# Optimization experiments

Hardware: AMD Instinct MI355X
Metric: run time of the kernel (lower is better)

The kernel has to match this reference:

```python
import jax, jax.numpy as jnp
import numpy as np

B, NUM_TAGS, SEQ_LEN, HIDDEN = 8, 1024, 4096, 256
BLOCK = SEQ_LEN // NUM_TAGS  # tokens per tag block


def setup_inputs() -> dict:
    key = jax.random.key(0)
    k1, k2 = jax.random.split(key)
    inputs = jax.random.normal(k1, (B, SEQ_LEN, HIDDEN), dtype=jnp.float32)
    # Structured tag->token mask: tag i covers token block i and (overlapping) block i+1,
    # mimicking nested HTML tags; the suffix-subtraction in the module resolves overlaps.
    tag_idx = jnp.arange(NUM_TAGS)[:, None]           # [T,1]
    tok_blk = jnp.arange(SEQ_LEN)[None, :] // BLOCK   # [1,S]
    mask = ((tok_blk == tag_idx) | (tok_blk == tag_idx + 1)).astype(jnp.float32)
    tag_to_token = jnp.broadcast_to(mask, (B, NUM_TAGS, SEQ_LEN))
    seq_emb = jax.random.normal(k2, (NUM_TAGS, HIDDEN), dtype=jnp.float32) * 0.02
    return {"inputs": inputs, "tag_to_token": tag_to_token, "seq_emb": seq_emb}


def _deduce_direct_string(tag_to_token):
    # Binary indicator of positive entries
    binm = (tag_to_token > 0).astype(tag_to_token.dtype)          # [B,T,S]
    # Exclusive suffix sum over the tag axis (rows below i), replacing the Python loop
    suffix_incl = jnp.flip(jnp.cumsum(jnp.flip(binm, axis=1), axis=1), axis=1)
    temp = binm - (suffix_incl - binm)                            # bin[i] - sum_{j>i} bin[j]
    temp = jnp.maximum(temp, 0.0)                                 # temp[temp<=0]=0
    # Row-normalize over tokens; empty rows divide by 1
    s = jnp.sum(temp, axis=2, keepdims=True)
    return temp / jnp.where(s == 0, 1.0, s)


def reference(inputs, tag_to_token, seq_emb):
    modified = _deduce_direct_string(tag_to_token)                # [B,T,S]
    out = jnp.einsum('bts,bsh->bth', modified, inputs)            # [B,T,H]
    num_tags = out.shape[1]
    return out + seq_emb[None, :num_tags, :]
```

## Files before the change

### kernel.cpp

```cpp
#include <hip/hip_runtime.h>

#define B_ 8
#define T_ 1024
#define S_ 4096
#define H_ 256

#define STRIP 64
#define CHUNK 128

__global__ void __launch_bounds__(256) colmax_pipe_kernel(const float* __restrict__ ttt,
                                                          int* __restrict__ L,
                                                          int2* __restrict__ range) {
    __shared__ unsigned long long wmask[2][4];
    __shared__ int red[4][STRIP];
    const int strippos = blockIdx.x >> 3;
    const int b  = blockIdx.x & 7;
    const int s0 = strippos * STRIP;
    const int w    = threadIdx.x >> 6;
    const int lane = threadIdx.x & 63;

    const float* colbase = ttt + (size_t)b * T_ * S_ + s0 + lane;

    int best = -1;
    int par = 0;
    float v[32], vn[32];

    {
        const float* p = colbase + (size_t)(T_ - CHUNK + w * 32) * S_;
#pragma unroll
        for (int j = 0; j < 32; ++j)
            v[j] = p[(size_t)j * S_];
    }

    for (int thi = T_; thi > 0; thi -= CHUNK) {
        const int t0 = thi - CHUNK + w * 32;
        if (thi > CHUNK) {
            const float* pn = colbase + (size_t)(t0 - CHUNK) * S_;
#pragma unroll
            for (int j = 0; j < 32; ++j)
                vn[j] = pn[(size_t)j * S_];
        }
        int lm = -1;
#pragma unroll
        for (int j = 0; j < 32; ++j)
            if (v[j] > 0.0f) lm = t0 + j;
        best = max(best, lm);

        wmask[par][w] = __ballot(best >= 0);
        __syncthreads();
        unsigned long long all = wmask[par][0] | wmask[par][1]
                               | wmask[par][2] | wmask[par][3];
        if (all == ~0ull) break;
        par ^= 1;
#pragma unroll
        for (int j = 0; j < 32; ++j)
            v[j] = vn[j];
    }

    red[w][lane] = best;
    __syncthreads();
    if (threadIdx.x < STRIP) {
        const int tid = threadIdx.x;
        int m = max(max(red[0][tid], red[1][tid]),
                    max(red[2][tid], red[3][tid]));
        L[b * S_ + s0 + tid] = m;
        int mn = (m < 0) ? 0x7fffffff : m;
        int mx = m;
#pragma unroll
        for (int k = 32; k >= 1; k >>= 1) {
            mn = min(mn, __shfl_xor(mn, k));
            mx = max(mx, __shfl_xor(mx, k));
        }
        if (tid == 0) {
            int2 rg = {mn, mx};
            range[b * (S_ / STRIP) + strippos] = rg;
        }
    }
}

__global__ void __launch_bounds__(256) gather_range_kernel(const float* __restrict__ inputs,
                                                           const int* __restrict__ L,
                                                           const int2* __restrict__ range,
                                                           const float* __restrict__ seq_emb,
                                                           float* __restrict__ out) {
    const int wid  = threadIdx.x >> 6;
    const int lane = threadIdx.x & 63;
    const int bt = blockIdx.x * 4 + wid;
    const int b = bt >> 10;
    const int t = bt & (T_ - 1);

    const float4* in4 = reinterpret_cast<const float4*>(inputs);

    int2 rg = range[b * (S_ / STRIP) + lane];
    unsigned long long smask = __ballot(rg.x <= t && t <= rg.y);

    float4 acc = {0.0f, 0.0f, 0.0f, 0.0f};
    int c = 0;

    while (smask) {
        int strip = __ffsll(smask) - 1; smask &= smask - 1;
        int Lv = L[b * S_ + strip * STRIP + lane];
        unsigned long long bm = __ballot(Lv == t);
        while (bm) {
            int l = __ffsll(bm) - 1; bm &= bm - 1;
            int s = strip * STRIP + l;
            float4 r = in4[(size_t)(b * S_ + s) * (H_ / 4) + lane];
            acc.x += r.x; acc.y += r.y; acc.z += r.z; acc.w += r.w; c++;
        }
    }

    float inv = (c > 0) ? (1.0f / (float)c) : 0.0f;
    float4 e = reinterpret_cast<const float4*>(seq_emb)[t * (H_ / 4) + lane];
    float4 o;
    o.x = acc.x * inv + e.x;
    o.y = acc.y * inv + e.y;
    o.z = acc.z * inv + e.z;
    o.w = acc.w * inv + e.w;
    reinterpret_cast<float4*>(out)[(size_t)bt * (H_ / 4) + lane] = o;
}

extern "C" void kernel_launch(void* const* d_in, const int* in_sizes, int n_in,
                              void* d_out, int out_size, void* d_ws, size_t ws_size,
                              hipStream_t stream) {
    const float* inputs  = (const float*)d_in[0];
    const float* ttt     = (const float*)d_in[1];
    const float* seq_emb = (const float*)d_in[2];
    float* out = (float*)d_out;

    int* L = (int*)d_ws;
    int2* range = (int2*)(L + B_ * S_);

    colmax_pipe_kernel<<<B_ * (S_ / STRIP), 256, 0, stream>>>(ttt, L, range);

    gather_range_kernel<<<B_ * T_ / 4, 256, 0, stream>>>(inputs, L, range, seq_emb, out);
}
```

Measured before the change: 28.57 us.

## Fuse column-max and gather kernels with inter-block flag synchronization

Merges the column-scan kernel and the gather kernel into a single launch of 512 blocks. Each block first computes last-positive-tag indices for one strip and publishes the strip range, then sets a per-block flag with release semantics. It then waits on the flags of all strips for its batch before gathering 16 output rows. This removes a kernel launch and the dependency gap between the two kernels. In exchange it relies on all blocks being co-resident, or it deadlocks. The flags are never reset, so on repeated calls the wait passes at once and can read stale L and range values from the previous call.

```diff
diff --git a/kernel.cpp b/kernel.cpp
--- a/kernel.cpp
+++ b/kernel.cpp
@@ -7,116 +7,140 @@
 
 #define STRIP 64
 #define CHUNK 128
+#define NSTRIP (S_ / STRIP)
+#define MAGICF 0x5F3759DFu
 
-__global__ void __launch_bounds__(256) colmax_pipe_kernel(const float* __restrict__ ttt,
-                                                          int* __restrict__ L,
-                                                          int2* __restrict__ range) {
+__global__ void __launch_bounds__(256) fused_flag_kernel(
+    const float* __restrict__ inputs,
+    const float* __restrict__ ttt,
+    const float* __restrict__ seq_emb,
+    float* __restrict__ out,
+    int* __restrict__ L,
+    int2* __restrict__ range,
+    unsigned int* __restrict__ flag) {
+
     __shared__ unsigned long long wmask[2][4];
     __shared__ int red[4][STRIP];
-    const int strippos = blockIdx.x >> 3;
-    const int b  = blockIdx.x & 7;
-    const int s0 = strippos * STRIP;
     const int w    = threadIdx.x >> 6;
     const int lane = threadIdx.x & 63;
 
-    const float* colbase = ttt + (size_t)b * T_ * S_ + s0 + lane;
+    {
+        const int strippos = blockIdx.x >> 3;
+        const int b  = blockIdx.x & 7;
+        const int s0 = strippos * STRIP;
+        const float* colbase = ttt + (size_t)b * T_ * S_ + s0 + lane;
 
-    int best = -1;
-    int par = 0;
-    float v[32], vn[32];
+        int best = -1;
+        int par = 0;
+        float v[32], vn[32];
 
-    {
-        const float* p = colbase + (size_t)(T_ - CHUNK + w * 32) * S_;
+        {
+            const float* p = colbase + (size_t)(T_ - CHUNK + w * 32) * S_;
 #pragma unroll
-        for (int j = 0; j < 32; ++j)
-            v[j] = p[(size_t)j * S_];
-    }
+            for (int j = 0; j < 32; ++j) v[j] = p[(size_t)j * S_];
+        }
 
-    for (int thi = T_; thi > 0; thi -= CHUNK) {
-        const int t0 = thi - CHUNK + w * 32;
-        if (thi > CHUNK) {
-            const float* pn = colbase + (size_t)(t0 - CHUNK) * S_;
+        for (int thi = T_; thi > 0; thi -= CHUNK) {
+            const int t0 = thi - CHUNK + w * 32;
+            if (thi > CHUNK) {
+                const float* pn = colbase + (size_t)(t0 - CHUNK) * S_;
+#pragma unroll
+                for (int j = 0; j < 32; ++j) vn[j] = pn[(size_t)j * S_];
+            }
+            int lm = -1;
 #pragma unroll
             for (int j = 0; j < 32; ++j)
-                vn[j] = pn[(size_t)j * S_];
+                if (v[j] > 0.0f) lm = t0 + j;
+            best = max(best, lm);
+
+            wmask[par][w] = __ballot(best >= 0);
+            __syncthreads();
+            unsigned long long all = wmask[par][0] | wmask[par][1]
+                                   | wmask[par][2] | wmask[par][3];
+            if (all == ~0ull) break;
+            par ^= 1;
+#pragma unroll
+            for (int j = 0; j < 32; ++j) v[j] = vn[j];
         }
-        int lm = -1;
+
+        red[w][lane] = best;
+        __syncthreads();
+        if (threadIdx.x < STRIP) {
+            const int tid = threadIdx.x;
+            int m = max(max(red[0][tid], red[1][tid]),
+                        max(red[2][tid], red[3][tid]));
+            L[b * S_ + s0 + tid] = m;
+            int mn = (m < 0) ? 0x7fffffff : m;
+            int mx = m;
 #pragma unroll
-        for (int j = 0; j < 32; ++j)
-            if (v[j] > 0.0f) lm = t0 + j;
-        best = max(best, lm);
-
-        wmask[par][w] = __ballot(best >= 0);
-        __syncthreads();
-        unsigned long long all = wmask[par][0] | wmask[par][1]
-                               | wmask[par][2] | wmask[par][3];
-        if (all == ~0ull) break;
-        par ^= 1;
-#pragma unroll
-        for (int j = 0; j < 32; ++j)
-            v[j] = vn[j];
-    }
-
-    red[w][lane] = best;
-    __syncthreads();
-    if (threadIdx.x < STRIP) {
-        const int tid = threadIdx.x;
-        int m = max(max(red[0][tid], red[1][tid]),
-                    max(red[2][tid], red[3][tid]));
-        L[b * S_ + s0 + tid] = m;
-        int mn = (m < 0) ? 0x7fffffff : m;
-        int mx = m;
-#pragma unroll
-        for (int k = 32; k >= 1; k >>= 1) {
-            mn = min(mn, __shfl_xor(mn, k));
-            mx = max(mx, __shfl_xor(mx, k));
-        }
-        if (tid == 0) {
-            int2 rg = {mn, mx};
-            range[b * (S_ / STRIP) + strippos] = rg;
-        }
-    }
-}
-
-__global__ void __launch_bounds__(256) gather_range_kernel(const float* __restrict__ inputs,
-                                                           const int* __restrict__ L,
-                                                           const int2* __restrict__ range,
-                                                           const float* __restrict__ seq_emb,
-                                                           float* __restrict__ out) {
-    const int wid  = threadIdx.x >> 6;
-    const int lane = threadIdx.x & 63;
-    const int bt = blockIdx.x * 4 + wid;
-    const int b = bt >> 10;
-    const int t = bt & (T_ - 1);
-
-    const float4* in4 = reinterpret_cast<const float4*>(inputs);
-
-    int2 rg = range[b * (S_ / STRIP) + lane];
-    unsigned long long smask = __ballot(rg.x <= t && t <= rg.y);
-
-    float4 acc = {0.0f, 0.0f, 0.0f, 0.0f};
-    int c = 0;
-
-    while (smask) {
-        int strip = __ffsll(smask) - 1; smask &= smask - 1;
-        int Lv = L[b * S_ + strip * STRIP + lane];
-        unsigned long long bm = __ballot(Lv == t);
-        while (bm) {
-            int l = __ffsll(bm) - 1; bm &= bm - 1;
-            int s = strip * STRIP + l;
-            float4 r = in4[(size_t)(b * S_ + s) * (H_ / 4) + lane];
-            acc.x += r.x; acc.y += r.y; acc.z += r.z; acc.w += r.w; c++;
+            for (int k = 32; k >= 1; k >>= 1) {
+                mn = min(mn, __shfl_xor(mn, k));
+                mx = max(mx, __shfl_xor(mx, k));
+            }
+            if (tid == 0) {
+                int2 rg = {mn, mx};
+                range[b * NSTRIP + strippos] = rg;
+                __threadfence();
+                atomicExch(&flag[blockIdx.x], MAGICF);
+            }
         }
     }
 
-    float inv = (c > 0) ? (1.0f / (float)c) : 0.0f;
-    float4 e = reinterpret_cast<const float4*>(seq_emb)[t * (H_ / 4) + lane];
-    float4 o;
-    o.x = acc.x * inv + e.x;
-    o.y = acc.y * inv + e.y;
-    o.z = acc.z * inv + e.z;
-    o.w = acc.w * inv + e.w;
-    reinterpret_cast<float4*>(out)[(size_t)bt * (H_ / 4) + lane] = o;
+    {
+        const int bt_base = blockIdx.x * 16;
+        const int b2 = bt_base >> 10;
+
+        {
+            const int sid = lane * 8 + b2;
+            while (__hip_atomic_load(&flag[sid], __ATOMIC_ACQUIRE,
+                                     __HIP_MEMORY_SCOPE_AGENT) != MAGICF)
+                __builtin_amdgcn_s_sleep(8);
+        }
+
+        int2 rg;
+        {
+            unsigned long long rr = __hip_atomic_load(
+                (const unsigned long long*)&range[b2 * NSTRIP + lane],
+                __ATOMIC_RELAXED, __HIP_MEMORY_SCOPE_AGENT);
+            rg.x = (int)(unsigned int)(rr & 0xffffffffull);
+            rg.y = (int)(unsigned int)(rr >> 32);
+        }
+
+        const float4* in4 = reinterpret_cast<const float4*>(inputs);
+
+        for (int r = 0; r < 4; ++r) {
+            const int bt = bt_base + w * 4 + r;
+            const int t = bt & (T_ - 1);
+
+            unsigned long long smask = __ballot(rg.x <= t && t <= rg.y);
+            float4 acc = {0.0f, 0.0f, 0.0f, 0.0f};
+            int c = 0;
+
+            while (smask) {
+                int strip = __ffsll(smask) - 1; smask &= smask - 1;
+                int Lv = __hip_atomic_load(&L[b2 * S_ + strip * STRIP + lane],
+                                           __ATOMIC_RELAXED,
+                                           __HIP_MEMORY_SCOPE_AGENT);
+                unsigned long long bm = __ballot(Lv == t);
+                while (bm) {
+                    int l = __ffsll(bm) - 1; bm &= bm - 1;
+                    int s = strip * STRIP + l;
+                    float4 rr4 = in4[(size_t)(b2 * S_ + s) * (H_ / 4) + lane];
+                    acc.x += rr4.x; acc.y += rr4.y;
+                    acc.z += rr4.z; acc.w += rr4.w; c++;
+                }
+            }
+
+            float inv = (c > 0) ? (1.0f / (float)c) : 0.0f;
+            float4 e = reinterpret_cast<const float4*>(seq_emb)[t * (H_ / 4) + lane];
+            float4 o;
+            o.x = acc.x * inv + e.x;
+            o.y = acc.y * inv + e.y;
+            o.z = acc.z * inv + e.z;
+            o.w = acc.w * inv + e.w;
+            reinterpret_cast<float4*>(out)[(size_t)bt * (H_ / 4) + lane] = o;
+        }
+    }
 }
 
 extern "C" void kernel_launch(void* const* d_in, const int* in_sizes, int n_in,
@@ -129,8 +153,8 @@
 
     int* L = (int*)d_ws;
     int2* range = (int2*)(L + B_ * S_);
+    unsigned int* flag = (unsigned int*)(range + B_ * NSTRIP);
 
-    colmax_pipe_kernel<<<B_ * (S_ / STRIP), 256, 0, stream>>>(ttt, L, range);
-
-    gather_range_kernel<<<B_ * T_ / 4, 256, 0, stream>>>(inputs, L, range, seq_emb, out);
+    fused_flag_kernel<<<B_ * NSTRIP, 256, 0, stream>>>(
+        inputs, ttt, seq_emb, out, L, range, flag);
 }
```

New measurement: 61.16 us. 2.14x slower.
